# Optimization experiments

Measured on AMD Instinct MI355X. Metric: run time of the kernel, lower is better.

Reference implementation:

```python
import jax, jax.numpy as jnp
import numpy as np
from jax import lax

B, N, C = 8, 16384, 128
HEADS, FF, KS = 8, 3.0, 5
HD = C // HEADS

def setup_inputs() -> dict:
    key = jax.random.key(0)
    ks = jax.random.split(key, 10)
    r = lambda k, s, sc=0.02: jax.random.normal(k, s, dtype=jnp.float32) * sc
    return {
        "x": jax.random.normal(ks[0], (B, N, C), dtype=jnp.float32),
        "Wq": r(ks[1], (C, C)),
        "Wkv": r(ks[2], (C, C)),
        "Wproj": r(ks[3], (C, C)),
        "bproj": jnp.zeros((C,), jnp.float32),
        "w_g": jax.random.normal(ks[4], (C, 1), dtype=jnp.float32),
        "scale": r(ks[5], (1, 1, C), 0.1),
        "pos_enc": r(ks[6], (1, N, C), 0.02),
        "dwc_w": r(ks[7], (HD, 1, KS, KS), 0.1),
        "dwc_b": jnp.zeros((HD,), jnp.float32),
        "H": 128,
        "W": 128,
    }

def _l2(a, axis):
    return jnp.sqrt(jnp.sum(a * a, axis=axis, keepdims=True))

def reference(x, Wq, Wkv, Wproj, bproj, w_g, scale, pos_enc, dwc_w, dwc_b, H, W):
    b, n_tok, c = x.shape
    scale_factor = HD ** (-0.5)
    q = x @ Wq.T                      # (B,N,C)
    k = x @ Wkv.T + pos_enc           # (B,N,C)  sr_ratio=1 path
    s = jax.nn.softplus(scale)
    q = (jax.nn.relu(q) + 1e-6) / s
    k = (jax.nn.relu(k) + 1e-6) / s
    qn, kn = _l2(q, -1), _l2(k, -1)
    q = q ** FF
    k = k ** FF
    q = q / _l2(q, -1) * qn
    k = k / _l2(k, -1) * kn
    A = (q @ w_g) * scale_factor      # (B,N,1)
    A = A / jnp.maximum(_l2(A, 1), 1e-12)  # F.normalize over dim=1
    G = jnp.sum(A * q, axis=1)        # (B,C)
    xg = G[:, None, :] * k            # (B,N,C)
    qh = q.reshape(b, n_tok, HEADS, HD).transpose(0, 2, 1, 3)  # (B,h,N,d)
    kh = k.reshape(b, n_tok, HEADS, HD).transpose(0, 2, 1, 3)
    z = 1.0 / (jnp.einsum('bhnd,bhd->bhn', qh, kh.mean(axis=2)) + 1e-6)
    xh = xg.reshape(b, n_tok, HEADS, HD).transpose(0, 2, 1, 3) * z[..., None]
    xo = xh.transpose(0, 2, 1, 3).reshape(b, n_tok, c)
    # faithful second transpose+reshape (memory reinterpretation in the source)
    xo = xo.transpose(0, 2, 1).reshape(b, n_tok, c)
    kimg = kh.reshape(b * HEADS, H, W, HD).transpose(0, 3, 1, 2)  # (B*h,d,H,W)
    pad = KS // 2
    conv = lax.conv_general_dilated(kimg, dwc_w, (1, 1), [(pad, pad), (pad, pad)],
                                    dimension_numbers=('NCHW', 'OIHW', 'NCHW'),
                                    feature_group_count=HD)
    conv = conv + dwc_b[None, :, None, None]
    xo = xo + conv.reshape(b, c, n_tok).transpose(0, 2, 1)
    return xo @ Wproj.T + bproj
```

## Files before the change

kernel.cpp:

```cpp
#include <hip/hip_runtime.h>
#include <hip/hip_bf16.h>

#define BB 8
#define NN 16384
#define CC 128

typedef __attribute__((ext_vector_type(8))) short bf16x8;
typedef __attribute__((ext_vector_type(4))) short short4v;
typedef __attribute__((ext_vector_type(4))) float f32x4;

__device__ __forceinline__ unsigned short f2bf(float f) {
    union { float f; unsigned u; } v; v.f = f;
    unsigned r = v.u + 0x7fffu + ((v.u >> 16) & 1u);
    return (unsigned short)(r >> 16);
}
__device__ __forceinline__ float bf2f(unsigned short h) {
    union { unsigned u; float f; } v; v.u = ((unsigned)h) << 16;
    return v.f;
}
__device__ __forceinline__ void split_trunc(float f, short& hi, short& lo) {
    union { float f; unsigned u; } v; v.f = f;
    const unsigned short hu = (unsigned short)(v.u >> 16);
    union { unsigned u; float f; } hf; hf.u = ((unsigned)hu) << 16;
    union { float f; unsigned u; } r; r.f = f - hf.f;
    hi = (short)hu;
    lo = (short)(r.u >> 16);
}

__global__ __launch_bounds__(256) void wprep_kernel(
    const float* __restrict__ Wq, const float* __restrict__ Wkv,
    const float* __restrict__ Wp, const float* __restrict__ scale,
    unsigned short* __restrict__ whi, unsigned short* __restrict__ wlo,
    float* __restrict__ sps)
{
    const int bid = blockIdx.x;
    if (bid == 48) {
        if (threadIdx.x < 128)
            sps[threadIdx.x] = 1.f / log1pf(expf(scale[threadIdx.x]));
        return;
    }
    const int mat = bid >> 4;
    const float* src = (mat == 0) ? Wq : ((mat == 1) ? Wkv : Wp);
    const int off = (bid & 15) * 1024 + threadIdx.x * 4;
    const float4 v = *(const float4*)(src + off);
    float f[4] = {v.x, v.y, v.z, v.w};
    short4v hv, lv;
#pragma unroll
    for (int j = 0; j < 4; ++j) {
        short h, lo2;
        split_trunc(f[j], h, lo2);
        hv[j] = h; lv[j] = lo2;
    }
    *(short4v*)(whi + mat * 16384 + off) = hv;
    *(short4v*)(wlo + mat * 16384 + off) = lv;
}

__global__ __launch_bounds__(256, 2) void qproj_kernel(
    const float* __restrict__ x, const unsigned short* __restrict__ whi,
    const unsigned short* __restrict__ wlo, const float* __restrict__ w_g,
    const float* __restrict__ sps,
    unsigned short* __restrict__ qout, float* __restrict__ partial1)
{
    __shared__ __align__(16) char wsm[65536];
    __shared__ float wpart[4][132];
    __shared__ float apl[128];

    const int tid  = threadIdx.x;
    const int w    = tid >> 6;
    const int l    = tid & 63;
    const int blk  = blockIdx.x;
    const int tok0 = blk * 128;

    bf16x8 xh[2][4], xl[2][4];
#pragma unroll
    for (int n = 0; n < 2; ++n) {
        const int r = w * 32 + n * 16 + (l & 15);
        const float* rowp = x + (tok0 + r) * 128 + (l >> 4) * 8;
#pragma unroll
        for (int kt = 0; kt < 4; ++kt) {
            const f32x4 a = *(const f32x4*)(rowp + kt * 32);
            const f32x4 b = *(const f32x4*)(rowp + kt * 32 + 4);
            const float f[8] = {a[0], a[1], a[2], a[3], b[0], b[1], b[2], b[3]};
            bf16x8 hv, lv;
#pragma unroll
            for (int j = 0; j < 8; ++j) {
                short h, lo2;
                split_trunc(f[j], h, lo2);
                hv[j] = h; lv[j] = lo2;
            }
            xh[n][kt] = hv; xl[n][kt] = lv;
        }
    }

#pragma unroll
    for (int it = 0; it < 16; ++it) {
        const int flat = it * 256 + tid;
        const int arr  = flat >> 11;
        const int c    = (flat >> 4) & 127;
        const int g    = flat & 15;
        const unsigned short* src = (arr ? wlo : whi) + c * 128 + g * 8;
        const int dst = arr * 32768 + c * 256 + ((g * 16) ^ ((c & 7) << 4));
        *(bf16x8*)(wsm + dst) = *(const bf16x8*)src;
    }
    __syncthreads();

    const int crow = (l >> 4) * 4;
    f32x4 acc[8][2];
#pragma unroll
    for (int m = 0; m < 8; ++m)
#pragma unroll
        for (int n = 0; n < 2; ++n) acc[m][n] = (f32x4)0.f;

#pragma unroll
    for (int m = 0; m < 8; ++m) {
        const int c = m * 16 + (l & 15);
        const int sw = (c & 7) << 4;
        bf16x8 ah[4], al[4];
#pragma unroll
        for (int kt = 0; kt < 4; ++kt) {
            const int fo = c * 256 + ((kt * 64 + (l >> 4) * 16) ^ sw);
            ah[kt] = *(const bf16x8*)(wsm + fo);
            al[kt] = *(const bf16x8*)(wsm + 32768 + fo);
        }
#pragma unroll
        for (int n = 0; n < 2; ++n)
#pragma unroll
            for (int kt = 0; kt < 4; ++kt) {
                acc[m][n] = __builtin_amdgcn_mfma_f32_16x16x32_bf16(ah[kt], xh[n][kt], acc[m][n], 0, 0, 0);
                acc[m][n] = __builtin_amdgcn_mfma_f32_16x16x32_bf16(ah[kt], xl[n][kt], acc[m][n], 0, 0, 0);
                acc[m][n] = __builtin_amdgcn_mfma_f32_16x16x32_bf16(al[kt], xh[n][kt], acc[m][n], 0, 0, 0);
            }
    }
    __syncthreads();

#pragma unroll
    for (int m = 0; m < 8; ++m) {
        const float4 is4 = *(const float4*)(sps + m * 16 + crow);
        const float is[4] = {is4.x, is4.y, is4.z, is4.w};
#pragma unroll
        for (int n = 0; n < 2; ++n)
#pragma unroll
            for (int j = 0; j < 4; ++j)
                acc[m][n][j] = (fmaxf(acc[m][n][j], 0.f) + 1e-6f) * is[j];
    }
    float fqn[2];
#pragma unroll
    for (int n = 0; n < 2; ++n) {
        float s2 = 0.f, s6 = 0.f;
#pragma unroll
        for (int m = 0; m < 8; ++m)
#pragma unroll
            for (int j = 0; j < 4; ++j) {
                const float v = acc[m][n][j], v2 = v * v;
                s2 += v2; s6 += v2 * v2 * v2;
            }
        s2 += __shfl_xor(s2, 16); s6 += __shfl_xor(s6, 16);
        s2 += __shfl_xor(s2, 32); s6 += __shfl_xor(s6, 32);
        fqn[n] = sqrtf(s2 / s6);
    }
#pragma unroll
    for (int m = 0; m < 8; ++m)
#pragma unroll
        for (int n = 0; n < 2; ++n)
#pragma unroll
            for (int j = 0; j < 4; ++j) {
                const float v = acc[m][n][j];
                acc[m][n][j] = v * v * v * fqn[n];
            }
    float d0 = 0.f, d1 = 0.f;
#pragma unroll
    for (int m = 0; m < 8; ++m) {
        const float4 wgv = *(const float4*)(w_g + m * 16 + crow);
#pragma unroll
        for (int j = 0; j < 4; ++j) {
            const float wg = (j == 0) ? wgv.x : (j == 1) ? wgv.y : (j == 2) ? wgv.z : wgv.w;
            d0 += acc[m][0][j] * wg;
            d1 += acc[m][1][j] * wg;
        }
    }
    d0 += __shfl_xor(d0, 16); d0 += __shfl_xor(d0, 32);
    d1 += __shfl_xor(d1, 16); d1 += __shfl_xor(d1, 32);
    const float ap0 = 0.25f * d0, ap1 = 0.25f * d1;

    float ssa = ap0 * ap0 + ap1 * ap1;
    ssa += __shfl_xor(ssa, 1); ssa += __shfl_xor(ssa, 2);
    ssa += __shfl_xor(ssa, 4); ssa += __shfl_xor(ssa, 8);
    if (l == 0) wpart[w][128] = ssa;
    if (l < 16) { apl[w * 32 + l] = ap0; apl[w * 32 + 16 + l] = ap1; }

    float g4[4] = {0.f, 0.f, 0.f, 0.f};
#pragma unroll
    for (int n = 0; n < 2; ++n) {
        const int t = l & 15;
        const int rb = w * 8192 + t * 512;
#pragma unroll
        for (int m = 0; m < 8; ++m) {
            const int ad = rb + (((m * 16 + crow) * 4) ^ ((t & 7) << 4));
            *(f32x4*)(wsm + ad) = acc[m][n];
        }
        asm volatile("s_waitcnt lgkmcnt(0)" ::: "memory");
#pragma unroll
        for (int j = 0; j < 8; ++j) {
            const int fid = j * 64 + l;
            const int row = fid >> 5;
            const int c4  = fid & 31;
            const int rb3 = w * 8192 + row * 512;
            const f32x4 v = *(f32x4*)(wsm + rb3 + ((c4 * 16) ^ ((row & 7) << 4)));
            const float apv = apl[w * 32 + n * 16 + row];
            short4v qv;
#pragma unroll
            for (int i = 0; i < 4; ++i) {
                g4[i] += apv * v[i];
                qv[i] = (short)f2bf(v[i]);
            }
            *(short4v*)(qout + (tok0 + w * 32 + n * 16 + row) * 128 + c4 * 4) = qv;
        }
    }
#pragma unroll
    for (int i = 0; i < 4; ++i) g4[i] += __shfl_xor(g4[i], 32);
    if (l < 32) {
#pragma unroll
        for (int i = 0; i < 4; ++i) wpart[w][(l & 31) * 4 + i] = g4[i];
    }
    __syncthreads();
    float* pblk = partial1 + blk * 132;
    if (tid < 128)
        pblk[tid] = wpart[0][tid] + wpart[1][tid] + wpart[2][tid] + wpart[3][tid];
    else if (tid == 128)
        pblk[128] = wpart[0][128] + wpart[1][128] + wpart[2][128] + wpart[3][128];
}

__global__ __launch_bounds__(256, 2) void kproj_kernel(
    const float* __restrict__ x, const unsigned short* __restrict__ whi,
    const unsigned short* __restrict__ wlo,
    const float* __restrict__ sps, const float* __restrict__ pos_enc,
    unsigned short* __restrict__ ktout, float* __restrict__ partial2)
{
    __shared__ __align__(16) char wsm[65536];
    __shared__ float wpart[4][128];

    const int tid  = threadIdx.x;
    const int w    = tid >> 6;
    const int l    = tid & 63;
    const int blk  = blockIdx.x;
    const int tok0 = blk * 128;
    const int tokb = (blk & 127) * 128;

    bf16x8 xh[2][4], xl[2][4];
#pragma unroll
    for (int n = 0; n < 2; ++n) {
        const int r = w * 32 + n * 16 + (l & 15);
        const float* rowp = x + (tok0 + r) * 128 + (l >> 4) * 8;
#pragma unroll
        for (int kt = 0; kt < 4; ++kt) {
            const f32x4 a = *(const f32x4*)(rowp + kt * 32);
            const f32x4 b = *(const f32x4*)(rowp + kt * 32 + 4);
            const float f[8] = {a[0], a[1], a[2], a[3], b[0], b[1], b[2], b[3]};
            bf16x8 hv, lv;
#pragma unroll
            for (int j = 0; j < 8; ++j) {
                short h, lo2;
                split_trunc(f[j], h, lo2);
                hv[j] = h; lv[j] = lo2;
            }
            xh[n][kt] = hv; xl[n][kt] = lv;
        }
    }

#pragma unroll
    for (int it = 0; it < 16; ++it) {
        const int flat = it * 256 + tid;
        const int arr  = flat >> 11;
        const int c    = (flat >> 4) & 127;
        const int g    = flat & 15;
        const unsigned short* src = (arr ? wlo : whi) + 16384 + c * 128 + g * 8;
        const int dst = arr * 32768 + c * 256 + ((g * 16) ^ ((c & 7) << 4));
        *(bf16x8*)(wsm + dst) = *(const bf16x8*)src;
    }
    __syncthreads();

    const int crow = (l >> 4) * 4;
    f32x4 acc[8][2];
#pragma unroll
    for (int m = 0; m < 8; ++m)
#pragma unroll
        for (int n = 0; n < 2; ++n) acc[m][n] = (f32x4)0.f;

#pragma unroll
    for (int m = 0; m < 8; ++m) {
        const int c = m * 16 + (l & 15);
        const int sw = (c & 7) << 4;
        bf16x8 ah[4], al[4];
#pragma unroll
        for (int kt = 0; kt < 4; ++kt) {
            const int fo = c * 256 + ((kt * 64 + (l >> 4) * 16) ^ sw);
            ah[kt] = *(const bf16x8*)(wsm + fo);
            al[kt] = *(const bf16x8*)(wsm + 32768 + fo);
        }
#pragma unroll
        for (int n = 0; n < 2; ++n)
#pragma unroll
            for (int kt = 0; kt < 4; ++kt) {
                acc[m][n] = __builtin_amdgcn_mfma_f32_16x16x32_bf16(ah[kt], xh[n][kt], acc[m][n], 0, 0, 0);
                acc[m][n] = __builtin_amdgcn_mfma_f32_16x16x32_bf16(ah[kt], xl[n][kt], acc[m][n], 0, 0, 0);
                acc[m][n] = __builtin_amdgcn_mfma_f32_16x16x32_bf16(al[kt], xh[n][kt], acc[m][n], 0, 0, 0);
            }
    }
    __syncthreads();

#pragma unroll
    for (int m = 0; m < 8; ++m) {
        const float4 is4 = *(const float4*)(sps + m * 16 + crow);
        const float is[4] = {is4.x, is4.y, is4.z, is4.w};
#pragma unroll
        for (int n = 0; n < 2; ++n) {
            const int t = tokb + w * 32 + n * 16 + (l & 15);
            const float4 p = *(const float4*)(pos_enc + t * 128 + m * 16 + crow);
            const float pe[4] = {p.x, p.y, p.z, p.w};
#pragma unroll
            for (int j = 0; j < 4; ++j)
                acc[m][n][j] = (fmaxf(acc[m][n][j] + pe[j], 0.f) + 1e-6f) * is[j];
        }
    }
    float fkn[2];
#pragma unroll
    for (int n = 0; n < 2; ++n) {
        float s2 = 0.f, s6 = 0.f;
#pragma unroll
        for (int m = 0; m < 8; ++m)
#pragma unroll
            for (int j = 0; j < 4; ++j) {
                const float v = acc[m][n][j], v2 = v * v;
                s2 += v2; s6 += v2 * v2 * v2;
            }
        s2 += __shfl_xor(s2, 16); s6 += __shfl_xor(s6, 16);
        s2 += __shfl_xor(s2, 32); s6 += __shfl_xor(s6, 32);
        fkn[n] = sqrtf(s2 / s6);
    }
#pragma unroll
    for (int m = 0; m < 8; ++m)
#pragma unroll
        for (int n = 0; n < 2; ++n)
#pragma unroll
            for (int j = 0; j < 4; ++j) {
                const float v = acc[m][n][j];
                acc[m][n][j] = v * v * v * fkn[n];
            }
#pragma unroll
    for (int m = 0; m < 8; ++m)
#pragma unroll
        for (int j = 0; j < 4; ++j) {
            float s = acc[m][0][j] + acc[m][1][j];
            s += __shfl_xor(s, 1); s += __shfl_xor(s, 2);
            s += __shfl_xor(s, 4); s += __shfl_xor(s, 8);
            if ((l & 15) == 0) wpart[w][m * 16 + crow + j] = s;
        }

#pragma unroll
    for (int m = 0; m < 8; ++m)
#pragma unroll
        for (int n = 0; n < 2; ++n)
#pragma unroll
            for (int j = 0; j < 4; ++j) {
                const int ch = m * 16 + crow + j;
                const int tl = w * 32 + n * 16 + (l & 15);
                *(unsigned short*)(wsm + ch * 264 + tl * 2) = f2bf(acc[m][n][j]);
            }
    __syncthreads();
    {
        const int bb = blk >> 7;
        unsigned* ktp = (unsigned*)ktout;
#pragma unroll
        for (int it = 0; it < 32; ++it) {
            const int idx = it * 256 + tid;
            const int row = idx >> 6;
            const int col = idx & 63;
            const unsigned v = *(unsigned*)(wsm + row * 264 + col * 4);
            ktp[(size_t)(bb * 128 + row) * 8192 + (blk & 127) * 64 + col] = v;
        }
    }
    __syncthreads();
    if (tid < 128)
        partial2[blk * 128 + tid] = wpart[0][tid] + wpart[1][tid] +
                                    wpart[2][tid] + wpart[3][tid];
}

__global__ __launch_bounds__(256) void reduce_kernel(
    const float* __restrict__ partial1, const float* __restrict__ partial2,
    float* __restrict__ G, float* __restrict__ kbar)
{
    const int b = blockIdx.x;
    const int tid = threadIdx.x;
    __shared__ float tmp[4];

    float ssa = (tid < 128) ? partial1[(b * 128 + tid) * 132 + 128] : 0.f;
#pragma unroll
    for (int o = 32; o >= 1; o >>= 1) ssa += __shfl_xor(ssa, o);
    if ((tid & 63) == 0) tmp[tid >> 6] = ssa;
    __syncthreads();
    const float anorm = fmaxf(sqrtf(tmp[0] + tmp[1] + tmp[2] + tmp[3]), 1e-12f);
    const float inv_a = 1.f / anorm;

    if (tid < 128) {
        float g = 0.f;
        for (int t = 0; t < 128; ++t)
            g += partial1[(b * 128 + t) * 132 + tid];
        G[b * 128 + tid] = g * inv_a;
    } else {
        const int c2 = tid - 128;
        float s = 0.f;
        for (int t = 0; t < 128; ++t)
            s += partial2[(b * 128 + t) * 128 + c2];
        kbar[b * 128 + c2] = s * (1.f / 16384.f);
    }
}

__global__ __launch_bounds__(256) void z_kernel(
    const unsigned short* __restrict__ q, const float* __restrict__ kbar,
    float* __restrict__ z)
{
    const int bid = blockIdx.x;
    const int b   = bid >> 8;
    const int tg  = bid & 255;
    const int tid = threadIdx.x;
    const int t   = tid >> 2;
    const int qt  = tid & 3;
    const int tok = tg * 64 + t;

    const unsigned short* qp = q + ((size_t)b * NN + tok) * 128 + qt * 32;
    const float* kb = kbar + b * 128 + qt * 32;

    float dot0 = 0.f, dot1 = 0.f;
#pragma unroll
    for (int c = 0; c < 4; ++c) {
        const short4v q4a = *(const short4v*)(qp + c * 8);
        const short4v q4b = *(const short4v*)(qp + c * 8 + 4);
        const float4 k4a = *(const float4*)(kb + c * 8);
        const float4 k4b = *(const float4*)(kb + c * 8 + 4);
        float d = bf2f((unsigned short)q4a[0]) * k4a.x + bf2f((unsigned short)q4a[1]) * k4a.y +
                  bf2f((unsigned short)q4a[2]) * k4a.z + bf2f((unsigned short)q4a[3]) * k4a.w +
                  bf2f((unsigned short)q4b[0]) * k4b.x + bf2f((unsigned short)q4b[1]) * k4b.y +
                  bf2f((unsigned short)q4b[2]) * k4b.z + bf2f((unsigned short)q4b[3]) * k4b.w;
        if (c < 2) dot0 += d; else dot1 += d;
    }
    z[((size_t)b * 8 + qt * 2) * NN + tok]     = 1.f / (dot0 + 1e-6f);
    z[((size_t)b * 8 + qt * 2 + 1) * NN + tok] = 1.f / (dot1 + 1e-6f);
}

__global__ __launch_bounds__(256, 2) void scp_kernel(
    float* __restrict__ out, const unsigned short* __restrict__ kt,
    const float* __restrict__ z, const float* __restrict__ G,
    const unsigned short* __restrict__ whi, const unsigned short* __restrict__ wlo,
    const float* __restrict__ bp, const float* __restrict__ dwc_w,
    const float* __restrict__ dwc_b)
{
    __shared__ __align__(16) char smem[32768];
    __shared__ float wct[25][16];
    __shared__ float bi[16];
    __shared__ float Gs;

    const int tid  = threadIdx.x;
    const int bid0 = blockIdx.x;
    const int bid  = (bid0 & 7) * 128 + (bid0 >> 3);
    const int cc   = bid & 127;
    const int b    = bid >> 7;
    const int n0   = bid * 128;

    for (int i = tid; i < 400; i += 256)
        wct[i >> 4][i & 15] = dwc_w[(i & 15) * 25 + (i >> 4)];
    if (tid < 16) bi[tid] = dwc_b[tid];
    if (tid == 0) Gs = G[b * 128 + cc];
    __syncthreads();

    const int ch4 = tid >> 3;
    const int xg  = tid & 7;

    float acc[4][16];
#pragma unroll
    for (int c = 0; c < 4; ++c)
#pragma unroll
        for (int i = 0; i < 16; ++i) acc[c][i] = 0.f;

#pragma unroll
    for (int dy = 0; dy < 5; ++dy) {
        const int yy = cc + dy - 2;
        if (yy < 0 || yy > 127) continue;
#pragma unroll
        for (int c = 0; c < 4; ++c) {
            const int ch = ch4 * 4 + c;
            const unsigned short* rowp = kt + ((size_t)b * 128 + ch) * NN
                                            + yy * 128 + xg * 16 - 8;
            float wf[32];
#pragma unroll
            for (int q4 = 0; q4 < 4; ++q4) {
                const bf16x8 v = *(const bf16x8*)(rowp + q4 * 8);
#pragma unroll
                for (int e = 0; e < 8; ++e)
                    wf[q4 * 8 + e] = bf2f((unsigned short)v[e]);
            }
            if (xg == 0) {
#pragma unroll
                for (int e = 0; e < 8; ++e) wf[e] = 0.f;
            }
            if (xg == 7) {
#pragma unroll
                for (int e = 24; e < 32; ++e) wf[e] = 0.f;
            }
            const int d = ch & 15;
#pragma unroll
            for (int dx = 0; dx < 5; ++dx) {
                const float wv = wct[dy * 5 + dx][d];
#pragma unroll
                for (int i = 0; i < 16; ++i)
                    acc[c][i] += wv * wf[i + dx + 6];
            }
        }
    }

    const float Gcc = Gs;
    const unsigned short* kub = kt + ((size_t)b * 128 + cc) * NN;
    const float* zr = z + ((size_t)b * 8 + (cc >> 4)) * NN;
    const int dbase = (ch4 & 3) * 4;
    const float4 b4 = *(const float4*)(&bi[dbase]);
    const float bv[4] = {b4.x, b4.y, b4.z, b4.w};
#pragma unroll
    for (int i = 0; i < 16; ++i) {
        const int r = xg * 16 + i;
        const int toks = r * 128 + ch4 * 4;
        const short4v ku4 = *(const short4v*)(kub + toks);
        const float4 z4 = *(const float4*)(zr + toks);
        const float zz[4] = {z4.x, z4.y, z4.z, z4.w};
        short4v hv;
#pragma unroll
        for (int c = 0; c < 4; ++c) {
            const float f = Gcc * bf2f((unsigned short)ku4[c]) * zz[c] + acc[c][i] + bv[c];
            hv[c] = (short)f2bf(f);
        }
        const int swz = (((r & 7) ^ ((r >> 3) & 7)) << 4);
        const int ad = r * 256 + (((ch4 >> 1) * 16) ^ swz) + (ch4 & 1) * 8;
        *(short4v*)(smem + ad) = hv;
    }
    __syncthreads();

    const int w  = tid >> 6;
    const int ll = tid & 63;
    bf16x8 xh[2][4];
    {
        const int lg16 = (ll >> 4) * 16;
#pragma unroll
        for (int n = 0; n < 2; ++n) {
            const int r = w * 32 + n * 16 + (ll & 15);
            const int rb = r * 256;
            const int swz = (((r & 7) ^ ((r >> 3) & 7)) << 4);
#pragma unroll
            for (int kt2 = 0; kt2 < 4; ++kt2)
                xh[n][kt2] = *(bf16x8*)(smem + rb + ((kt2 * 64 + lg16) ^ swz));
        }
    }
    const int crow = (ll >> 4) * 4;
    f32x4 pacc[8][2];
#pragma unroll
    for (int m = 0; m < 8; ++m)
#pragma unroll
        for (int n = 0; n < 2; ++n) pacc[m][n] = (f32x4)0.f;

#pragma unroll
    for (int m = 0; m < 8; ++m) {
        const int c = m * 16 + (ll & 15);
        bf16x8 ah[4], al[4];
#pragma unroll
        for (int kt2 = 0; kt2 < 4; ++kt2) {
            const int off = 32768 + c * 128 + kt2 * 32 + (ll >> 4) * 8;
            ah[kt2] = *(const bf16x8*)(whi + off);
            al[kt2] = *(const bf16x8*)(wlo + off);
        }
#pragma unroll
        for (int n = 0; n < 2; ++n)
#pragma unroll
            for (int kt2 = 0; kt2 < 4; ++kt2) {
                pacc[m][n] = __builtin_amdgcn_mfma_f32_16x16x32_bf16(ah[kt2], xh[n][kt2], pacc[m][n], 0, 0, 0);
                pacc[m][n] = __builtin_amdgcn_mfma_f32_16x16x32_bf16(al[kt2], xh[n][kt2], pacc[m][n], 0, 0, 0);
            }
    }

#pragma unroll
    for (int m = 0; m < 8; ++m) {
        const float4 bq = *(const float4*)(bp + m * 16 + crow);
        const float bb[4] = {bq.x, bq.y, bq.z, bq.w};
#pragma unroll
        for (int n = 0; n < 2; ++n)
#pragma unroll
            for (int j = 0; j < 4; ++j) pacc[m][n][j] += bb[j];
    }
    __syncthreads();
#pragma unroll
    for (int n = 0; n < 2; ++n) {
        const int t = ll & 15;
        const int rb = w * 8192 + t * 512;
#pragma unroll
        for (int m = 0; m < 8; ++m) {
            const int ad = rb + (((m * 16 + crow) * 4) ^ ((t & 7) << 4));
            *(f32x4*)(smem + ad) = pacc[m][n];
        }
        asm volatile("s_waitcnt lgkmcnt(0)" ::: "memory");
#pragma unroll
        for (int j = 0; j < 8; ++j) {
            const int fid = j * 64 + ll;
            const int row = fid >> 5;
            const int c4  = fid & 31;
            const int rb3 = w * 8192 + row * 512;
            const f32x4 v = *(f32x4*)(smem + rb3 + ((c4 * 16) ^ ((row & 7) << 4)));
            *(f32x4*)(out + (n0 + w * 32 + n * 16 + row) * 128 + c4 * 4) = v;
        }
    }
}

extern "C" void kernel_launch(void* const* d_in, const int* in_sizes, int n_in,
                              void* d_out, int out_size, void* d_ws, size_t ws_size,
                              hipStream_t stream)
{
    const float* x       = (const float*)d_in[0];
    const float* Wq      = (const float*)d_in[1];
    const float* Wkv     = (const float*)d_in[2];
    const float* Wproj   = (const float*)d_in[3];
    const float* bproj   = (const float*)d_in[4];
    const float* w_g     = (const float*)d_in[5];
    const float* scale   = (const float*)d_in[6];
    const float* pos_enc = (const float*)d_in[7];
    const float* dwc_w   = (const float*)d_in[8];
    const float* dwc_b   = (const float*)d_in[9];
    float* out = (float*)d_out;

    char* ws = (char*)d_ws;
    unsigned short* qbuf = (unsigned short*)(ws);
    unsigned short* ktbuf= (unsigned short*)(ws + 33554432);
    float* partial1 = (float*)(ws + 67108864);
    float* partial2 = (float*)(ws + 67649536);
    float* G        = (float*)(ws + 68173824);
    float* kbar     = (float*)(ws + 68177920);
    unsigned short* whi = (unsigned short*)(ws + 68182016);
    unsigned short* wlo = (unsigned short*)(ws + 68280320);
    float* sps      = (float*)(ws + 68378624);
    float* zbuf     = (float*)(ws + 68379136);

    wprep_kernel<<<dim3(49), dim3(256), 0, stream>>>(
        Wq, Wkv, Wproj, scale, whi, wlo, sps);
    qproj_kernel<<<dim3(1024), dim3(256), 0, stream>>>(
        x, whi, wlo, w_g, sps, qbuf, partial1);
    kproj_kernel<<<dim3(1024), dim3(256), 0, stream>>>(
        x, whi, wlo, sps, pos_enc, ktbuf, partial2);
    reduce_kernel<<<dim3(8), dim3(256), 0, stream>>>(
        partial1, partial2, G, kbar);
    z_kernel<<<dim3(2048), dim3(256), 0, stream>>>(qbuf, kbar, zbuf);
    scp_kernel<<<dim3(1024), dim3(256), 0, stream>>>(
        out, ktbuf, zbuf, G, whi, wlo, bproj, dwc_w, dwc_b);
}
```

Before: 170.3 us.

## Reorder k before q projection and fuse z computation into q projection

Runs the k projection and the k-mean reduction first, so the q projection kernel can compute z directly from its registers using kbar. This removes the bf16 q buffer write (32 MB) and the separate z kernel that reread it, and the G partials are now reduced with cross-lane shuffles instead of an LDS transpose. In exchange there is an extra small reduce launch, plus many shuffle reductions in the q kernel.

```diff
diff --git a/kernel.cpp b/kernel.cpp
--- a/kernel.cpp
+++ b/kernel.cpp
@@ -55,21 +55,190 @@
     *(short4v*)(wlo + mat * 16384 + off) = lv;
 }
 
-__global__ __launch_bounds__(256, 2) void qproj_kernel(
+__global__ __launch_bounds__(256, 2) void kproj_kernel(
     const float* __restrict__ x, const unsigned short* __restrict__ whi,
-    const unsigned short* __restrict__ wlo, const float* __restrict__ w_g,
-    const float* __restrict__ sps,
-    unsigned short* __restrict__ qout, float* __restrict__ partial1)
+    const unsigned short* __restrict__ wlo,
+    const float* __restrict__ sps, const float* __restrict__ pos_enc,
+    unsigned short* __restrict__ ktout, float* __restrict__ partial2)
 {
     __shared__ __align__(16) char wsm[65536];
-    __shared__ float wpart[4][132];
-    __shared__ float apl[128];
+    __shared__ float wpart[4][128];
 
     const int tid  = threadIdx.x;
     const int w    = tid >> 6;
     const int l    = tid & 63;
     const int blk  = blockIdx.x;
     const int tok0 = blk * 128;
+    const int tokb = (blk & 127) * 128;
+
+    bf16x8 xh[2][4], xl[2][4];
+#pragma unroll
+    for (int n = 0; n < 2; ++n) {
+        const int r = w * 32 + n * 16 + (l & 15);
+        const float* rowp = x + (tok0 + r) * 128 + (l >> 4) * 8;
+#pragma unroll
+        for (int kt = 0; kt < 4; ++kt) {
+            const f32x4 a = *(const f32x4*)(rowp + kt * 32);
+            const f32x4 b = *(const f32x4*)(rowp + kt * 32 + 4);
+            const float f[8] = {a[0], a[1], a[2], a[3], b[0], b[1], b[2], b[3]};
+            bf16x8 hv, lv;
+#pragma unroll
+            for (int j = 0; j < 8; ++j) {
+                short h, lo2;
+                split_trunc(f[j], h, lo2);
+                hv[j] = h; lv[j] = lo2;
+            }
+            xh[n][kt] = hv; xl[n][kt] = lv;
+        }
+    }
+
+#pragma unroll
+    for (int it = 0; it < 16; ++it) {
+        const int flat = it * 256 + tid;
+        const int arr  = flat >> 11;
+        const int c    = (flat >> 4) & 127;
+        const int g    = flat & 15;
+        const unsigned short* src = (arr ? wlo : whi) + 16384 + c * 128 + g * 8;
+        const int dst = arr * 32768 + c * 256 + ((g * 16) ^ ((c & 7) << 4));
+        *(bf16x8*)(wsm + dst) = *(const bf16x8*)src;
+    }
+    __syncthreads();
+
+    const int crow = (l >> 4) * 4;
+    f32x4 acc[8][2];
+#pragma unroll
+    for (int m = 0; m < 8; ++m)
+#pragma unroll
+        for (int n = 0; n < 2; ++n) acc[m][n] = (f32x4)0.f;
+
+#pragma unroll
+    for (int m = 0; m < 8; ++m) {
+        const int c = m * 16 + (l & 15);
+        const int sw = (c & 7) << 4;
+        bf16x8 ah[4], al[4];
+#pragma unroll
+        for (int kt = 0; kt < 4; ++kt) {
+            const int fo = c * 256 + ((kt * 64 + (l >> 4) * 16) ^ sw);
+            ah[kt] = *(const bf16x8*)(wsm + fo);
+            al[kt] = *(const bf16x8*)(wsm + 32768 + fo);
+        }
+#pragma unroll
+        for (int n = 0; n < 2; ++n)
+#pragma unroll
+            for (int kt = 0; kt < 4; ++kt) {
+                acc[m][n] = __builtin_amdgcn_mfma_f32_16x16x32_bf16(ah[kt], xh[n][kt], acc[m][n], 0, 0, 0);
+                acc[m][n] = __builtin_amdgcn_mfma_f32_16x16x32_bf16(ah[kt], xl[n][kt], acc[m][n], 0, 0, 0);
+                acc[m][n] = __builtin_amdgcn_mfma_f32_16x16x32_bf16(al[kt], xh[n][kt], acc[m][n], 0, 0, 0);
+            }
+    }
+    __syncthreads();
+
+#pragma unroll
+    for (int m = 0; m < 8; ++m) {
+        const float4 is4 = *(const float4*)(sps + m * 16 + crow);
+        const float is[4] = {is4.x, is4.y, is4.z, is4.w};
+#pragma unroll
+        for (int n = 0; n < 2; ++n) {
+            const int t = tokb + w * 32 + n * 16 + (l & 15);
+            const float4 p = *(const float4*)(pos_enc + t * 128 + m * 16 + crow);
+            const float pe[4] = {p.x, p.y, p.z, p.w};
+#pragma unroll
+            for (int j = 0; j < 4; ++j)
+                acc[m][n][j] = (fmaxf(acc[m][n][j] + pe[j], 0.f) + 1e-6f) * is[j];
+        }
+    }
+    float fkn[2];
+#pragma unroll
+    for (int n = 0; n < 2; ++n) {
+        float s2 = 0.f, s6 = 0.f;
+#pragma unroll
+        for (int m = 0; m < 8; ++m)
+#pragma unroll
+            for (int j = 0; j < 4; ++j) {
+                const float v = acc[m][n][j], v2 = v * v;
+                s2 += v2; s6 += v2 * v2 * v2;
+            }
+        s2 += __shfl_xor(s2, 16); s6 += __shfl_xor(s6, 16);
+        s2 += __shfl_xor(s2, 32); s6 += __shfl_xor(s6, 32);
+        fkn[n] = sqrtf(s2 / s6);
+    }
+#pragma unroll
+    for (int m = 0; m < 8; ++m)
+#pragma unroll
+        for (int n = 0; n < 2; ++n)
+#pragma unroll
+            for (int j = 0; j < 4; ++j) {
+                const float v = acc[m][n][j];
+                acc[m][n][j] = v * v * v * fkn[n];
+            }
+#pragma unroll
+    for (int m = 0; m < 8; ++m)
+#pragma unroll
+        for (int j = 0; j < 4; ++j) {
+            float s = acc[m][0][j] + acc[m][1][j];
+            s += __shfl_xor(s, 1); s += __shfl_xor(s, 2);
+            s += __shfl_xor(s, 4); s += __shfl_xor(s, 8);
+            if ((l & 15) == 0) wpart[w][m * 16 + crow + j] = s;
+        }
+
+#pragma unroll
+    for (int m = 0; m < 8; ++m)
+#pragma unroll
+        for (int n = 0; n < 2; ++n)
+#pragma unroll
+            for (int j = 0; j < 4; ++j) {
+                const int ch = m * 16 + crow + j;
+                const int tl = w * 32 + n * 16 + (l & 15);
+                *(unsigned short*)(wsm + ch * 264 + tl * 2) = f2bf(acc[m][n][j]);
+            }
+    __syncthreads();
+    {
+        const int bb = blk >> 7;
+        unsigned* ktp = (unsigned*)ktout;
+#pragma unroll
+        for (int it = 0; it < 32; ++it) {
+            const int idx = it * 256 + tid;
+            const int row = idx >> 6;
+            const int col = idx & 63;
+            const unsigned v = *(unsigned*)(wsm + row * 264 + col * 4);
+            ktp[(size_t)(bb * 128 + row) * 8192 + (blk & 127) * 64 + col] = v;
+        }
+    }
+    __syncthreads();
+    if (tid < 128)
+        partial2[blk * 128 + tid] = wpart[0][tid] + wpart[1][tid] +
+                                    wpart[2][tid] + wpart[3][tid];
+}
+
+__global__ __launch_bounds__(256) void reducek_kernel(
+    const float* __restrict__ partial2, float* __restrict__ kbar)
+{
+    const int b = blockIdx.x;
+    const int tid = threadIdx.x;
+    if (tid < 128) {
+        float s = 0.f;
+        for (int t = 0; t < 128; ++t)
+            s += partial2[(b * 128 + t) * 128 + tid];
+        kbar[b * 128 + tid] = s * (1.f / 16384.f);
+    }
+}
+
+__global__ __launch_bounds__(256, 2) void qproj_kernel(
+    const float* __restrict__ x, const unsigned short* __restrict__ whi,
+    const unsigned short* __restrict__ wlo, const float* __restrict__ w_g,
+    const float* __restrict__ sps, const float* __restrict__ kbar,
+    float* __restrict__ z, float* __restrict__ partial1)
+{
+    __shared__ __align__(16) char wsm[65536];
+    __shared__ float wpart[4][132];
+
+    const int tid  = threadIdx.x;
+    const int w    = tid >> 6;
+    const int l    = tid & 63;
+    const int blk  = blockIdx.x;
+    const int tok0 = blk * 128;
+    const int bq   = blk >> 7;
+    const int tokb = (blk & 127) * 128;
 
     bf16x8 xh[2][4], xl[2][4];
 #pragma unroll
@@ -131,7 +300,6 @@
                 acc[m][n] = __builtin_amdgcn_mfma_f32_16x16x32_bf16(al[kt], xh[n][kt], acc[m][n], 0, 0, 0);
             }
     }
-    __syncthreads();
 
 #pragma unroll
     for (int m = 0; m < 8; ++m) {
@@ -167,6 +335,26 @@
                 const float v = acc[m][n][j];
                 acc[m][n][j] = v * v * v * fqn[n];
             }
+
+#pragma unroll
+    for (int m = 0; m < 8; ++m) {
+        const float4 kb = *(const float4*)(kbar + bq * 128 + m * 16 + crow);
+        const float kbv[4] = {kb.x, kb.y, kb.z, kb.w};
+        float dm0 = 0.f, dm1 = 0.f;
+#pragma unroll
+        for (int j = 0; j < 4; ++j) {
+            dm0 += acc[m][0][j] * kbv[j];
+            dm1 += acc[m][1][j] * kbv[j];
+        }
+        dm0 += __shfl_xor(dm0, 16); dm0 += __shfl_xor(dm0, 32);
+        dm1 += __shfl_xor(dm1, 16); dm1 += __shfl_xor(dm1, 32);
+        if (l < 16) {
+            const int t0 = tokb + w * 32 + l;
+            z[((size_t)bq * 8 + m) * NN + t0]      = 1.f / (dm0 + 1e-6f);
+            z[((size_t)bq * 8 + m) * NN + t0 + 16] = 1.f / (dm1 + 1e-6f);
+        }
+    }
+
     float d0 = 0.f, d1 = 0.f;
 #pragma unroll
     for (int m = 0; m < 8; ++m) {
@@ -186,42 +374,16 @@
     ssa += __shfl_xor(ssa, 1); ssa += __shfl_xor(ssa, 2);
     ssa += __shfl_xor(ssa, 4); ssa += __shfl_xor(ssa, 8);
     if (l == 0) wpart[w][128] = ssa;
-    if (l < 16) { apl[w * 32 + l] = ap0; apl[w * 32 + 16 + l] = ap1; }
-
-    float g4[4] = {0.f, 0.f, 0.f, 0.f};
-#pragma unroll
-    for (int n = 0; n < 2; ++n) {
-        const int t = l & 15;
-        const int rb = w * 8192 + t * 512;
-#pragma unroll
-        for (int m = 0; m < 8; ++m) {
-            const int ad = rb + (((m * 16 + crow) * 4) ^ ((t & 7) << 4));
-            *(f32x4*)(wsm + ad) = acc[m][n];
-        }
-        asm volatile("s_waitcnt lgkmcnt(0)" ::: "memory");
-#pragma unroll
-        for (int j = 0; j < 8; ++j) {
-            const int fid = j * 64 + l;
-            const int row = fid >> 5;
-            const int c4  = fid & 31;
-            const int rb3 = w * 8192 + row * 512;
-            const f32x4 v = *(f32x4*)(wsm + rb3 + ((c4 * 16) ^ ((row & 7) << 4)));
-            const float apv = apl[w * 32 + n * 16 + row];
-            short4v qv;
-#pragma unroll
-            for (int i = 0; i < 4; ++i) {
-                g4[i] += apv * v[i];
-                qv[i] = (short)f2bf(v[i]);
-            }
-            *(short4v*)(qout + (tok0 + w * 32 + n * 16 + row) * 128 + c4 * 4) = qv;
-        }
-    }
-#pragma unroll
-    for (int i = 0; i < 4; ++i) g4[i] += __shfl_xor(g4[i], 32);
-    if (l < 32) {
-#pragma unroll
-        for (int i = 0; i < 4; ++i) wpart[w][(l & 31) * 4 + i] = g4[i];
-    }
+
+#pragma unroll
+    for (int m = 0; m < 8; ++m)
+#pragma unroll
+        for (int j = 0; j < 4; ++j) {
+            float g = ap0 * acc[m][0][j] + ap1 * acc[m][1][j];
+            g += __shfl_xor(g, 1); g += __shfl_xor(g, 2);
+            g += __shfl_xor(g, 4); g += __shfl_xor(g, 8);
+            if ((l & 15) == 0) wpart[w][m * 16 + crow + j] = g;
+        }
     __syncthreads();
     float* pblk = partial1 + blk * 132;
     if (tid < 128)
@@ -230,164 +392,8 @@
         pblk[128] = wpart[0][128] + wpart[1][128] + wpart[2][128] + wpart[3][128];
 }
 
-__global__ __launch_bounds__(256, 2) void kproj_kernel(
-    const float* __restrict__ x, const unsigned short* __restrict__ whi,
-    const unsigned short* __restrict__ wlo,
-    const float* __restrict__ sps, const float* __restrict__ pos_enc,
-    unsigned short* __restrict__ ktout, float* __restrict__ partial2)
-{
-    __shared__ __align__(16) char wsm[65536];
-    __shared__ float wpart[4][128];
-
-    const int tid  = threadIdx.x;
-    const int w    = tid >> 6;
-    const int l    = tid & 63;
-    const int blk  = blockIdx.x;
-    const int tok0 = blk * 128;
-    const int tokb = (blk & 127) * 128;
-
-    bf16x8 xh[2][4], xl[2][4];
-#pragma unroll
-    for (int n = 0; n < 2; ++n) {
-        const int r = w * 32 + n * 16 + (l & 15);
-        const float* rowp = x + (tok0 + r) * 128 + (l >> 4) * 8;
-#pragma unroll
-        for (int kt = 0; kt < 4; ++kt) {
-            const f32x4 a = *(const f32x4*)(rowp + kt * 32);
-            const f32x4 b = *(const f32x4*)(rowp + kt * 32 + 4);
-            const float f[8] = {a[0], a[1], a[2], a[3], b[0], b[1], b[2], b[3]};
-            bf16x8 hv, lv;
-#pragma unroll
-            for (int j = 0; j < 8; ++j) {
-                short h, lo2;
-                split_trunc(f[j], h, lo2);
-                hv[j] = h; lv[j] = lo2;
-            }
-            xh[n][kt] = hv; xl[n][kt] = lv;
-        }
-    }
-
-#pragma unroll
-    for (int it = 0; it < 16; ++it) {
-        const int flat = it * 256 + tid;
-        const int arr  = flat >> 11;
-        const int c    = (flat >> 4) & 127;
-        const int g    = flat & 15;
-        const unsigned short* src = (arr ? wlo : whi) + 16384 + c * 128 + g * 8;
-        const int dst = arr * 32768 + c * 256 + ((g * 16) ^ ((c & 7) << 4));
-        *(bf16x8*)(wsm + dst) = *(const bf16x8*)src;
-    }
-    __syncthreads();
-
-    const int crow = (l >> 4) * 4;
-    f32x4 acc[8][2];
-#pragma unroll
-    for (int m = 0; m < 8; ++m)
-#pragma unroll
-        for (int n = 0; n < 2; ++n) acc[m][n] = (f32x4)0.f;
-
-#pragma unroll
-    for (int m = 0; m < 8; ++m) {
-        const int c = m * 16 + (l & 15);
-        const int sw = (c & 7) << 4;
-        bf16x8 ah[4], al[4];
-#pragma unroll
-        for (int kt = 0; kt < 4; ++kt) {
-            const int fo = c * 256 + ((kt * 64 + (l >> 4) * 16) ^ sw);
-            ah[kt] = *(const bf16x8*)(wsm + fo);
-            al[kt] = *(const bf16x8*)(wsm + 32768 + fo);
-        }
-#pragma unroll
-        for (int n = 0; n < 2; ++n)
-#pragma unroll
-            for (int kt = 0; kt < 4; ++kt) {
-                acc[m][n] = __builtin_amdgcn_mfma_f32_16x16x32_bf16(ah[kt], xh[n][kt], acc[m][n], 0, 0, 0);
-                acc[m][n] = __builtin_amdgcn_mfma_f32_16x16x32_bf16(ah[kt], xl[n][kt], acc[m][n], 0, 0, 0);
-                acc[m][n] = __builtin_amdgcn_mfma_f32_16x16x32_bf16(al[kt], xh[n][kt], acc[m][n], 0, 0, 0);
-            }
-    }
-    __syncthreads();
-
-#pragma unroll
-    for (int m = 0; m < 8; ++m) {
-        const float4 is4 = *(const float4*)(sps + m * 16 + crow);
-        const float is[4] = {is4.x, is4.y, is4.z, is4.w};
-#pragma unroll
-        for (int n = 0; n < 2; ++n) {
-            const int t = tokb + w * 32 + n * 16 + (l & 15);
-            const float4 p = *(const float4*)(pos_enc + t * 128 + m * 16 + crow);
-            const float pe[4] = {p.x, p.y, p.z, p.w};
-#pragma unroll
-            for (int j = 0; j < 4; ++j)
-                acc[m][n][j] = (fmaxf(acc[m][n][j] + pe[j], 0.f) + 1e-6f) * is[j];
-        }
-    }
-    float fkn[2];
-#pragma unroll
-    for (int n = 0; n < 2; ++n) {
-        float s2 = 0.f, s6 = 0.f;
-#pragma unroll
-        for (int m = 0; m < 8; ++m)
-#pragma unroll
-            for (int j = 0; j < 4; ++j) {
-                const float v = acc[m][n][j], v2 = v * v;
-                s2 += v2; s6 += v2 * v2 * v2;
-            }
-        s2 += __shfl_xor(s2, 16); s6 += __shfl_xor(s6, 16);
-        s2 += __shfl_xor(s2, 32); s6 += __shfl_xor(s6, 32);
-        fkn[n] = sqrtf(s2 / s6);
-    }
-#pragma unroll
-    for (int m = 0; m < 8; ++m)
-#pragma unroll
-        for (int n = 0; n < 2; ++n)
-#pragma unroll
-            for (int j = 0; j < 4; ++j) {
-                const float v = acc[m][n][j];
-                acc[m][n][j] = v * v * v * fkn[n];
-            }
-#pragma unroll
-    for (int m = 0; m < 8; ++m)
-#pragma unroll
-        for (int j = 0; j < 4; ++j) {
-            float s = acc[m][0][j] + acc[m][1][j];
-            s += __shfl_xor(s, 1); s += __shfl_xor(s, 2);
-            s += __shfl_xor(s, 4); s += __shfl_xor(s, 8);
-            if ((l & 15) == 0) wpart[w][m * 16 + crow + j] = s;
-        }
-
-#pragma unroll
-    for (int m = 0; m < 8; ++m)
-#pragma unroll
-        for (int n = 0; n < 2; ++n)
-#pragma unroll
-            for (int j = 0; j < 4; ++j) {
-                const int ch = m * 16 + crow + j;
-                const int tl = w * 32 + n * 16 + (l & 15);
-                *(unsigned short*)(wsm + ch * 264 + tl * 2) = f2bf(acc[m][n][j]);
-            }
-    __syncthreads();
-    {
-        const int bb = blk >> 7;
-        unsigned* ktp = (unsigned*)ktout;
-#pragma unroll
-        for (int it = 0; it < 32; ++it) {
-            const int idx = it * 256 + tid;
-            const int row = idx >> 6;
-            const int col = idx & 63;
-            const unsigned v = *(unsigned*)(wsm + row * 264 + col * 4);
-            ktp[(size_t)(bb * 128 + row) * 8192 + (blk & 127) * 64 + col] = v;
-        }
-    }
-    __syncthreads();
-    if (tid < 128)
-        partial2[blk * 128 + tid] = wpart[0][tid] + wpart[1][tid] +
-                                    wpart[2][tid] + wpart[3][tid];
-}
-
-__global__ __launch_bounds__(256) void reduce_kernel(
-    const float* __restrict__ partial1, const float* __restrict__ partial2,
-    float* __restrict__ G, float* __restrict__ kbar)
+__global__ __launch_bounds__(256) void reduceg_kernel(
+    const float* __restrict__ partial1, float* __restrict__ G)
 {
     const int b = blockIdx.x;
     const int tid = threadIdx.x;
@@ -406,45 +412,7 @@
         for (int t = 0; t < 128; ++t)
             g += partial1[(b * 128 + t) * 132 + tid];
         G[b * 128 + tid] = g * inv_a;
-    } else {
-        const int c2 = tid - 128;
-        float s = 0.f;
-        for (int t = 0; t < 128; ++t)
-            s += partial2[(b * 128 + t) * 128 + c2];
-        kbar[b * 128 + c2] = s * (1.f / 16384.f);
-    }
-}
-
-__global__ __launch_bounds__(256) void z_kernel(
-    const unsigned short* __restrict__ q, const float* __restrict__ kbar,
-    float* __restrict__ z)
-{
-    const int bid = blockIdx.x;
-    const int b   = bid >> 8;
-    const int tg  = bid & 255;
-    const int tid = threadIdx.x;
-    const int t   = tid >> 2;
-    const int qt  = tid & 3;
-    const int tok = tg * 64 + t;
-
-    const unsigned short* qp = q + ((size_t)b * NN + tok) * 128 + qt * 32;
-    const float* kb = kbar + b * 128 + qt * 32;
-
-    float dot0 = 0.f, dot1 = 0.f;
-#pragma unroll
-    for (int c = 0; c < 4; ++c) {
-        const short4v q4a = *(const short4v*)(qp + c * 8);
-        const short4v q4b = *(const short4v*)(qp + c * 8 + 4);
-        const float4 k4a = *(const float4*)(kb + c * 8);
-        const float4 k4b = *(const float4*)(kb + c * 8 + 4);
-        float d = bf2f((unsigned short)q4a[0]) * k4a.x + bf2f((unsigned short)q4a[1]) * k4a.y +
-                  bf2f((unsigned short)q4a[2]) * k4a.z + bf2f((unsigned short)q4a[3]) * k4a.w +
-                  bf2f((unsigned short)q4b[0]) * k4b.x + bf2f((unsigned short)q4b[1]) * k4b.y +
-                  bf2f((unsigned short)q4b[2]) * k4b.z + bf2f((unsigned short)q4b[3]) * k4b.w;
-        if (c < 2) dot0 += d; else dot1 += d;
-    }
-    z[((size_t)b * 8 + qt * 2) * NN + tok]     = 1.f / (dot0 + 1e-6f);
-    z[((size_t)b * 8 + qt * 2 + 1) * NN + tok] = 1.f / (dot1 + 1e-6f);
+    }
 }
 
 __global__ __launch_bounds__(256, 2) void scp_kernel(
@@ -632,26 +600,24 @@
     float* out = (float*)d_out;
 
     char* ws = (char*)d_ws;
-    unsigned short* qbuf = (unsigned short*)(ws);
-    unsigned short* ktbuf= (unsigned short*)(ws + 33554432);
-    float* partial1 = (float*)(ws + 67108864);
-    float* partial2 = (float*)(ws + 67649536);
-    float* G        = (float*)(ws + 68173824);
-    float* kbar     = (float*)(ws + 68177920);
-    unsigned short* whi = (unsigned short*)(ws + 68182016);
-    unsigned short* wlo = (unsigned short*)(ws + 68280320);
-    float* sps      = (float*)(ws + 68378624);
-    float* zbuf     = (float*)(ws + 68379136);
+    float* partial1 = (float*)(ws);
+    float* partial2 = (float*)(ws + 540672);
+    float* G        = (float*)(ws + 1064960);
+    float* kbar     = (float*)(ws + 1069056);
+    unsigned short* whi = (unsigned short*)(ws + 1073152);
+    unsigned short* wlo = (unsigned short*)(ws + 1171456);
+    float* sps      = (float*)(ws + 1269760);
+    float* zbuf     = (float*)(ws + 1270272);
+    unsigned short* ktbuf = (unsigned short*)(ws + 5464576);
 
     wprep_kernel<<<dim3(49), dim3(256), 0, stream>>>(
         Wq, Wkv, Wproj, scale, whi, wlo, sps);
-    qproj_kernel<<<dim3(1024), dim3(256), 0, stream>>>(
-        x, whi, wlo, w_g, sps, qbuf, partial1);
     kproj_kernel<<<dim3(1024), dim3(256), 0, stream>>>(
         x, whi, wlo, sps, pos_enc, ktbuf, partial2);
-    reduce_kernel<<<dim3(8), dim3(256), 0, stream>>>(
-        partial1, partial2, G, kbar);
-    z_kernel<<<dim3(2048), dim3(256), 0, stream>>>(qbuf, kbar, zbuf);
+    reducek_kernel<<<dim3(8), dim3(256), 0, stream>>>(partial2, kbar);
+    qproj_kernel<<<dim3(1024), dim3(256), 0, stream>>>(
+        x, whi, wlo, w_g, sps, kbar, zbuf, partial1);
+    reduceg_kernel<<<dim3(8), dim3(256), 0, stream>>>(partial1, G);
     scp_kernel<<<dim3(1024), dim3(256), 0, stream>>>(
         out, ktbuf, zbuf, G, whi, wlo, bproj, dwc_w, dwc_b);
 }
```

Result: no change. 168.9 us, median of 2 (-0.8%).
